# Kernel tuning notes

Hardware: AMD Instinct MI355X
Metric: run time of the kernel (lower is better)

Reference implementation:

```python
import jax, jax.numpy as jnp
import numpy as np

NUM_HEADS = 12
QK_SCALE = 1.0
EPS = 1e-12  # torch.nn.functional.normalize default eps


def _l2norm(t):
    # matches torch F.normalize: x / max(||x||_2, eps) along last axis
    n = jnp.sqrt(jnp.sum(t * t, axis=-1, keepdims=True))
    return t / jnp.maximum(n, EPS)


def setup_inputs() -> dict:
    key = jax.random.key(0)
    k1, k2 = jax.random.split(key)
    B, N, dim = 8, 4096, 768
    x = jax.random.normal(k1, (B, N, 3 * dim), dtype=jnp.float32)
    temperature = jnp.ones((NUM_HEADS, 1, 1), dtype=jnp.float32)
    proj_w = jax.random.normal(k2, (dim, dim), dtype=jnp.float32) * (1.0 / np.sqrt(dim))
    proj_b = jnp.zeros((dim,), dtype=jnp.float32)
    return {"x": x, "temperature": temperature, "proj_w": proj_w, "proj_b": proj_b}


def reference(x, temperature, proj_w, proj_b):
    B, N, C3 = x.shape
    C = C3 // 3
    H = NUM_HEADS
    d = C // H
    # (B, N, 3, H, d) -> (3, B, H, N, d)
    qkv = x.reshape(B, N, 3, H, d).transpose(2, 0, 3, 1, 4)
    q, k, v = qkv[0], qkv[1], qkv[2]
    q = jnp.swapaxes(q, -2, -1) * QK_SCALE   # [B, H, d, N]
    v = jnp.swapaxes(v, -2, -1)              # [B, H, d, N]
    q = _l2norm(q)                           # normalize over tokens N
    k = _l2norm(k)                           # normalize over head dim d (k is [B,H,N,d])
    # cross-covariance attention over channels: [B, H, d, d]
    attn = jnp.einsum('bhdn,bhne->bhde', q, k) * temperature
    attn = jax.nn.softmax(attn, axis=-1)
    out = jnp.einsum('bhde,bhen->bhdn', attn, v)  # [B, H, d, N]
    out = out.transpose(0, 3, 1, 2).reshape(B, N, C)  # [B, N, C]
    out = out @ proj_w.T + proj_b
    return out
```

## Files before the change

### kernel.cpp

```cpp
#include <hip/hip_runtime.h>
#include <hip/hip_bf16.h>

#define BB 8
#define NN 4096
#define HH 12
#define CC 768
#define C3 2304

typedef float  f32x4  __attribute__((ext_vector_type(4)));
typedef __bf16 bf16x8 __attribute__((ext_vector_type(8)));

__global__ __launch_bounds__(256) void k1_logits(const float* __restrict__ x,
                                                 float* __restrict__ S,
                                                 float* __restrict__ qss) {
  const int slice = blockIdx.x, h = blockIdx.y, b = blockIdx.z;
  const int tid = threadIdx.x;
  __shared__ float qb[8][68];
  __shared__ float kb[8][68];
  __shared__ float invk[8];

  const int t8     = tid >> 5;
  const int lane32 = tid & 31;
  const bool isQ   = lane32 < 16;
  const int col4   = (lane32 & 15) * 4;
  const int i0     = tid >> 4;
  const int jc     = tid & 15;

  float acc[4][4];
#pragma unroll
  for (int r = 0; r < 4; ++r)
#pragma unroll
    for (int c = 0; c < 4; ++c) acc[r][c] = 0.f;
  float qsl[4] = {0.f, 0.f, 0.f, 0.f};

  for (int g = 0; g < 32; ++g) {
    const int n = slice * 256 + g * 8 + t8;
    const float* p = x + (size_t)(b * NN + n) * C3 + (isQ ? 0 : 768) + h * 64 + col4;
    const float4 v = *(const float4*)p;
    __syncthreads();
    if (isQ) *(float4*)&qb[t8][col4] = v;
    else     *(float4*)&kb[t8][col4] = v;
    __syncthreads();
    {
      const float a = kb[t8][lane32];
      const float c = kb[t8][lane32 + 32];
      float ps = a * a + c * c;
      ps += __shfl_xor(ps, 1);
      ps += __shfl_xor(ps, 2);
      ps += __shfl_xor(ps, 4);
      ps += __shfl_xor(ps, 8);
      ps += __shfl_xor(ps, 16);
      if (lane32 == 0) invk[t8] = 1.0f / fmaxf(sqrtf(ps), 1e-12f);
    }
    __syncthreads();
#pragma unroll
    for (int t = 0; t < 8; ++t) {
      const float inv = invk[t];
      float4 kv = *(const float4*)&kb[t][jc * 4];
      kv.x *= inv; kv.y *= inv; kv.z *= inv; kv.w *= inv;
#pragma unroll
      for (int r = 0; r < 4; ++r) {
        const float qv = qb[t][i0 + 16 * r];
        acc[r][0] = fmaf(qv, kv.x, acc[r][0]);
        acc[r][1] = fmaf(qv, kv.y, acc[r][1]);
        acc[r][2] = fmaf(qv, kv.z, acc[r][2]);
        acc[r][3] = fmaf(qv, kv.w, acc[r][3]);
        if (jc == 0) qsl[r] = fmaf(qv, qv, qsl[r]);
      }
    }
  }

  float* Sp = S + (size_t)(b * HH + h) * 4096;
#pragma unroll
  for (int r = 0; r < 4; ++r) {
    const int i = i0 + 16 * r;
#pragma unroll
    for (int c = 0; c < 4; ++c)
      atomicAdd(&Sp[i * 64 + jc * 4 + c], acc[r][c]);
    if (jc == 0) atomicAdd(&qss[(b * HH + h) * 64 + i], qsl[r]);
  }
}

__global__ __launch_bounds__(64) void k2_softmax(const float* __restrict__ S,
                                                 const float* __restrict__ qss,
                                                 const float* __restrict__ temp,
                                                 float* __restrict__ attn) {
  const int h = blockIdx.x, b = blockIdx.y;
  const int i = threadIdx.x;
  const size_t bh = (size_t)(b * HH + h);
  const float rqs = 1.0f / fmaxf(sqrtf(qss[bh * 64 + i]), 1e-12f);
  const float tp  = temp[h] * rqs;
  const float* Sp = S + bh * 4096 + i * 64;
  float v[64];
  float m = -3.4e38f;
#pragma unroll
  for (int j = 0; j < 64; ++j) { v[j] = Sp[j] * tp; m = fmaxf(m, v[j]); }
  float s = 0.f;
#pragma unroll
  for (int j = 0; j < 64; ++j) { v[j] = __expf(v[j] - m); s += v[j]; }
  const float inv = 1.0f / s;
  float* Ap = attn + bh * 4096 + i * 64;
#pragma unroll
  for (int j = 0; j < 64; ++j) Ap[j] = v[j] * inv;
}

__global__ __launch_bounds__(256) void k3_w2(const float* __restrict__ attn,
                                             const float* __restrict__ pw,
                                             __bf16* __restrict__ W2) {
  const int ct = blockIdx.x, h = blockIdx.y, b = blockIdx.z;
  const int co0 = ct * 64;
  __shared__ float pT[64][65];
  __shared__ float ab[64][64];
  const int tid = threadIdx.x;
  const int r = tid >> 2, c0 = (tid & 3) * 16;
  {
    const float* pp = pw + (size_t)(co0 + r) * CC + h * 64 + c0;
    const float4 p0 = *(const float4*)(pp + 0);
    const float4 p1 = *(const float4*)(pp + 4);
    const float4 p2 = *(const float4*)(pp + 8);
    const float4 p3 = *(const float4*)(pp + 12);
    const float* ap = attn + (size_t)(b * HH + h) * 4096 + r * 64 + c0;
    const float4 a0 = *(const float4*)(ap + 0);
    const float4 a1 = *(const float4*)(ap + 4);
    const float4 a2 = *(const float4*)(ap + 8);
    const float4 a3 = *(const float4*)(ap + 12);
    pT[c0 +  0][r] = p0.x; pT[c0 +  1][r] = p0.y; pT[c0 +  2][r] = p0.z; pT[c0 +  3][r] = p0.w;
    pT[c0 +  4][r] = p1.x; pT[c0 +  5][r] = p1.y; pT[c0 +  6][r] = p1.z; pT[c0 +  7][r] = p1.w;
    pT[c0 +  8][r] = p2.x; pT[c0 +  9][r] = p2.y; pT[c0 + 10][r] = p2.z; pT[c0 + 11][r] = p2.w;
    pT[c0 + 12][r] = p3.x; pT[c0 + 13][r] = p3.y; pT[c0 + 14][r] = p3.z; pT[c0 + 15][r] = p3.w;
    *(float4*)&ab[r][c0 + 0]  = a0;
    *(float4*)&ab[r][c0 + 4]  = a1;
    *(float4*)&ab[r][c0 + 8]  = a2;
    *(float4*)&ab[r][c0 + 12] = a3;
  }
  __syncthreads();
  const int col = tid & 63, jg = tid >> 6;
  float accJ[16];
#pragma unroll
  for (int c = 0; c < 16; ++c) accJ[c] = 0.f;
#pragma unroll 4
  for (int i = 0; i < 64; ++i) {
    const float p = pT[i][col];
    const float4* a4 = (const float4*)&ab[i][jg * 16];
    const float4 A0 = a4[0], A1 = a4[1], A2 = a4[2], A3 = a4[3];
    accJ[0]  = fmaf(p, A0.x, accJ[0]);  accJ[1]  = fmaf(p, A0.y, accJ[1]);
    accJ[2]  = fmaf(p, A0.z, accJ[2]);  accJ[3]  = fmaf(p, A0.w, accJ[3]);
    accJ[4]  = fmaf(p, A1.x, accJ[4]);  accJ[5]  = fmaf(p, A1.y, accJ[5]);
    accJ[6]  = fmaf(p, A1.z, accJ[6]);  accJ[7]  = fmaf(p, A1.w, accJ[7]);
    accJ[8]  = fmaf(p, A2.x, accJ[8]);  accJ[9]  = fmaf(p, A2.y, accJ[9]);
    accJ[10] = fmaf(p, A2.z, accJ[10]); accJ[11] = fmaf(p, A2.w, accJ[11]);
    accJ[12] = fmaf(p, A3.x, accJ[12]); accJ[13] = fmaf(p, A3.y, accJ[13]);
    accJ[14] = fmaf(p, A3.z, accJ[14]); accJ[15] = fmaf(p, A3.w, accJ[15]);
  }
  bf16x8 u0, u1;
#pragma unroll
  for (int c = 0; c < 8; ++c) { u0[c] = (__bf16)accJ[c]; u1[c] = (__bf16)accJ[8 + c]; }
  __bf16* wp = W2 + ((size_t)b * CC + co0 + col) * CC + h * 64 + jg * 16;
  *(bf16x8*)(wp)     = u0;
  *(bf16x8*)(wp + 8) = u1;
}

__global__ __launch_bounds__(256) void k4_gemm(const float* __restrict__ x,
                                               const __bf16* __restrict__ W2,
                                               const float* __restrict__ pb,
                                               float* __restrict__ out) {
  const int mt = blockIdx.x, nt = blockIdx.y, bz = blockIdx.z;
  const int m0 = mt * 128, co0 = nt * 128;
  __shared__ __bf16 At[128][40];
  __shared__ __bf16 Bt[128][40];
  const int tid  = threadIdx.x;
  const int w    = tid >> 6, lane = tid & 63;
  const int wm   = w >> 1,   wn   = w & 1;
  const int fr   = lane & 15;
  const int fk   = lane >> 4;

  f32x4 acc[4][4];
#pragma unroll
  for (int tm = 0; tm < 4; ++tm)
#pragma unroll
    for (int tn = 0; tn < 4; ++tn) acc[tm][tn] = (f32x4){0.f, 0.f, 0.f, 0.f};

  const int srow = tid >> 1, shalf = tid & 1;
  const float*  Ag = x  + (size_t)(bz * NN + m0 + srow) * C3 + 1536 + shalf * 16;
  const __bf16* Bg = W2 + ((size_t)bz * CC + co0 + srow) * CC + shalf * 16;

  for (int kk = 0; kk < 24; ++kk) {
    const int kb = kk * 32;
    const float4 a0 = *(const float4*)(Ag + kb + 0);
    const float4 a1 = *(const float4*)(Ag + kb + 4);
    const float4 a2 = *(const float4*)(Ag + kb + 8);
    const float4 a3 = *(const float4*)(Ag + kb + 12);
    const float4 bv0 = *(const float4*)(Bg + kb);
    const float4 bv1 = *(const float4*)(Bg + kb + 8);
    __syncthreads();
    bf16x8 ua, ub;
    ua[0] = (__bf16)a0.x; ua[1] = (__bf16)a0.y; ua[2] = (__bf16)a0.z; ua[3] = (__bf16)a0.w;
    ua[4] = (__bf16)a1.x; ua[5] = (__bf16)a1.y; ua[6] = (__bf16)a1.z; ua[7] = (__bf16)a1.w;
    ub[0] = (__bf16)a2.x; ub[1] = (__bf16)a2.y; ub[2] = (__bf16)a2.z; ub[3] = (__bf16)a2.w;
    ub[4] = (__bf16)a3.x; ub[5] = (__bf16)a3.y; ub[6] = (__bf16)a3.z; ub[7] = (__bf16)a3.w;
    *(bf16x8*)&At[srow][shalf * 16 + 0] = ua;
    *(bf16x8*)&At[srow][shalf * 16 + 8] = ub;
    *(float4*)&Bt[srow][shalf * 16 + 0] = bv0;
    *(float4*)&Bt[srow][shalf * 16 + 8] = bv1;
    __syncthreads();
    bf16x8 afr[4], bfr[4];
#pragma unroll
    for (int tm = 0; tm < 4; ++tm)
      afr[tm] = *(const bf16x8*)&At[wm * 64 + tm * 16 + fr][fk * 8];
#pragma unroll
    for (int tn = 0; tn < 4; ++tn)
      bfr[tn] = *(const bf16x8*)&Bt[wn * 64 + tn * 16 + fr][fk * 8];
#pragma unroll
    for (int tm = 0; tm < 4; ++tm)
#pragma unroll
      for (int tn = 0; tn < 4; ++tn)
        acc[tm][tn] = __builtin_amdgcn_mfma_f32_16x16x32_bf16(afr[tm], bfr[tn],
                                                              acc[tm][tn], 0, 0, 0);
  }

#pragma unroll
  for (int tn = 0; tn < 4; ++tn) {
    const int co = co0 + wn * 64 + tn * 16 + fr;
    const float bias = pb[co];
#pragma unroll
    for (int tm = 0; tm < 4; ++tm) {
#pragma unroll
      for (int rr = 0; rr < 4; ++rr) {
        const int row = m0 + wm * 64 + tm * 16 + fk * 4 + rr;
        out[(size_t)(bz * NN + row) * CC + co] = acc[tm][tn][rr] + bias;
      }
    }
  }
}

extern "C" void kernel_launch(void* const* d_in, const int* in_sizes, int n_in,
                              void* d_out, int out_size, void* d_ws, size_t ws_size,
                              hipStream_t stream) {
  const float* x    = (const float*)d_in[0];
  const float* temp = (const float*)d_in[1];
  const float* pw   = (const float*)d_in[2];
  const float* pb   = (const float*)d_in[3];
  float* out = (float*)d_out;
  char* ws = (char*)d_ws;

  float*  S    = (float*)(ws);
  float*  qss  = (float*)(ws + 1572864);
  float*  attn = (float*)(ws + 1597440);
  __bf16* W2   = (__bf16*)(ws + 3170304);

  hipMemsetAsync(ws, 0, 1597440, stream);

  hipLaunchKernelGGL(k1_logits,  dim3(16, 12, 8), dim3(256), 0, stream, x, S, qss);
  hipLaunchKernelGGL(k2_softmax, dim3(12, 8),     dim3(64),  0, stream, S, qss, temp, attn);
  hipLaunchKernelGGL(k3_w2,      dim3(12, 12, 8), dim3(256), 0, stream, attn, pw, W2);
  hipLaunchKernelGGL(k4_gemm,    dim3(32, 6, 8),  dim3(256), 0, stream, x, W2, pb, out);
}
```

Baseline: 615.6 us.

## Pre-convert V to bf16 and stream GEMM tiles via direct global-to-LDS loads

Adds a pre-pass kernel that converts the V slice of x to a packed bf16 buffer in workspace. The projection GEMM then loads A and B tiles with global_load_lds straight into unpadded LDS, instead of loading fp32, converting in registers and storing to LDS. It also remaps the 1D grid so groups of M tiles share each batch's W2 columns, for better L2 locality. The cost is an extra full read of V plus a bf16 write, and possible LDS bank conflicts now that the row padding is gone.

```diff
diff --git a/kernel.cpp b/kernel.cpp
--- a/kernel.cpp
+++ b/kernel.cpp
@@ -9,6 +9,23 @@
 
 typedef float  f32x4  __attribute__((ext_vector_type(4)));
 typedef __bf16 bf16x8 __attribute__((ext_vector_type(8)));
+typedef __bf16 bf16x4 __attribute__((ext_vector_type(4)));
+
+__device__ __forceinline__ void gload16(const void* g, void* l) {
+  __builtin_amdgcn_global_load_lds((const __attribute__((address_space(1))) void*)g,
+                                   (__attribute__((address_space(3))) void*)l, 16, 0, 0);
+}
+
+__global__ __launch_bounds__(256) void k0_vcvt(const float* __restrict__ x,
+                                               __bf16* __restrict__ vb) {
+  const int idx = blockIdx.x * 256 + threadIdx.x;
+  const int bn = idx / 192;
+  const int c4 = (idx - bn * 192) * 4;
+  const float4 v = *(const float4*)(x + (size_t)bn * C3 + 1536 + c4);
+  bf16x4 r;
+  r[0] = (__bf16)v.x; r[1] = (__bf16)v.y; r[2] = (__bf16)v.z; r[3] = (__bf16)v.w;
+  *(bf16x4*)(vb + (size_t)bn * CC + c4) = r;
+}
 
 __global__ __launch_bounds__(256) void k1_logits(const float* __restrict__ x,
                                                  float* __restrict__ S,
@@ -160,14 +177,22 @@
   *(bf16x8*)(wp + 8) = u1;
 }
 
-__global__ __launch_bounds__(256) void k4_gemm(const float* __restrict__ x,
+__global__ __launch_bounds__(256) void k4_gemm(const __bf16* __restrict__ vb,
                                                const __bf16* __restrict__ W2,
                                                const float* __restrict__ pb,
                                                float* __restrict__ out) {
-  const int mt = blockIdx.x, nt = blockIdx.y, bz = blockIdx.z;
+  int id = blockIdx.x;
+  const int bz = id / 192;
+  const int rem = id - bz * 192;
+  const int mg = rem / 48;
+  const int idx = rem - mg * 48;
+  const int nt = idx >> 3;
+  const int mt = mg * 8 + (idx & 7);
   const int m0 = mt * 128, co0 = nt * 128;
-  __shared__ __bf16 At[128][40];
-  __shared__ __bf16 Bt[128][40];
+
+  __shared__ __bf16 At[128][32];
+  __shared__ __bf16 Bt[128][32];
+
   const int tid  = threadIdx.x;
   const int w    = tid >> 6, lane = tid & 63;
   const int wm   = w >> 1,   wn   = w & 1;
@@ -180,28 +205,22 @@
 #pragma unroll
     for (int tn = 0; tn < 4; ++tn) acc[tm][tn] = (f32x4){0.f, 0.f, 0.f, 0.f};
 
-  const int srow = tid >> 1, shalf = tid & 1;
-  const float*  Ag = x  + (size_t)(bz * NN + m0 + srow) * C3 + 1536 + shalf * 16;
-  const __bf16* Bg = W2 + ((size_t)bz * CC + co0 + srow) * CC + shalf * 16;
+  const int srow = lane >> 2;
+  const int scol = (lane & 3) * 8;
+  const __bf16* Ag = vb + (size_t)(bz * NN + m0 + w * 32 + srow) * CC + scol;
+  const __bf16* Bg = W2 + ((size_t)bz * CC + co0 + w * 32 + srow) * CC + scol;
+  __bf16* lA0 = &At[w * 32][0];
+  __bf16* lA1 = &At[w * 32 + 16][0];
+  __bf16* lB0 = &Bt[w * 32][0];
+  __bf16* lB1 = &Bt[w * 32 + 16][0];
 
   for (int kk = 0; kk < 24; ++kk) {
     const int kb = kk * 32;
-    const float4 a0 = *(const float4*)(Ag + kb + 0);
-    const float4 a1 = *(const float4*)(Ag + kb + 4);
-    const float4 a2 = *(const float4*)(Ag + kb + 8);
-    const float4 a3 = *(const float4*)(Ag + kb + 12);
-    const float4 bv0 = *(const float4*)(Bg + kb);
-    const float4 bv1 = *(const float4*)(Bg + kb + 8);
-    __syncthreads();
-    bf16x8 ua, ub;
-    ua[0] = (__bf16)a0.x; ua[1] = (__bf16)a0.y; ua[2] = (__bf16)a0.z; ua[3] = (__bf16)a0.w;
-    ua[4] = (__bf16)a1.x; ua[5] = (__bf16)a1.y; ua[6] = (__bf16)a1.z; ua[7] = (__bf16)a1.w;
-    ub[0] = (__bf16)a2.x; ub[1] = (__bf16)a2.y; ub[2] = (__bf16)a2.z; ub[3] = (__bf16)a2.w;
-    ub[4] = (__bf16)a3.x; ub[5] = (__bf16)a3.y; ub[6] = (__bf16)a3.z; ub[7] = (__bf16)a3.w;
-    *(bf16x8*)&At[srow][shalf * 16 + 0] = ua;
-    *(bf16x8*)&At[srow][shalf * 16 + 8] = ub;
-    *(float4*)&Bt[srow][shalf * 16 + 0] = bv0;
-    *(float4*)&Bt[srow][shalf * 16 + 8] = bv1;
+    __syncthreads();
+    gload16(Ag + kb,            lA0);
+    gload16(Ag + 16 * CC + kb,  lA1);
+    gload16(Bg + kb,            lB0);
+    gload16(Bg + 16 * CC + kb,  lB1);
     __syncthreads();
     bf16x8 afr[4], bfr[4];
 #pragma unroll
@@ -247,11 +266,13 @@
   float*  qss  = (float*)(ws + 1572864);
   float*  attn = (float*)(ws + 1597440);
   __bf16* W2   = (__bf16*)(ws + 3170304);
+  __bf16* vb   = (__bf16*)(ws + 12607488);
 
   hipMemsetAsync(ws, 0, 1597440, stream);
 
+  hipLaunchKernelGGL(k0_vcvt,    dim3(24576),     dim3(256), 0, stream, x, vb);
   hipLaunchKernelGGL(k1_logits,  dim3(16, 12, 8), dim3(256), 0, stream, x, S, qss);
   hipLaunchKernelGGL(k2_softmax, dim3(12, 8),     dim3(64),  0, stream, S, qss, temp, attn);
   hipLaunchKernelGGL(k3_w2,      dim3(12, 12, 8), dim3(256), 0, stream, attn, pw, W2);
-  hipLaunchKernelGGL(k4_gemm,    dim3(32, 6, 8),  dim3(256), 0, stream, x, W2, pb, out);
-}
+  hipLaunchKernelGGL(k4_gemm,    dim3(1536),      dim3(256), 0, stream, vb, W2, pb, out);
+}
```

Result: no change. 615.5 us (-0.0%).
